# Kernel tuning notes

Measured on AMD Instinct MI355X. Metric: run time of the kernel, lower is better.

Reference implementation:

```python
import jax, jax.numpy as jnp
import numpy as np

BETA = 1.0 - 0.01      # 1 - voltage_decay
THRESH = 1.0           # threshold_voltage; theta state is never updated in the
                       # original forward (theta1/theta2 stay at init=0), so the
                       # effective adaptive threshold is THRESH + 0 every step.
ALPHA = 2.0            # snntorch default ATan surrogate alpha

@jax.custom_vjp
def spike_fn(x):
    # Heaviside forward, ATan surrogate backward (snntorch default spike_grad)
    return (x > 0).astype(x.dtype)

def _spike_fwd(x):
    return (x > 0).astype(x.dtype), x

def _spike_bwd(x, g):
    return (g * (ALPHA / 2.0) / (1.0 + (jnp.pi / 2.0 * ALPHA * x) ** 2),)

spike_fn.defvjp(_spike_fwd, _spike_bwd)

def setup_inputs() -> dict:
    key = jax.random.key(0)
    k0, k1, k2 = jax.random.split(key, 3)
    B, T, D, H, A = 128, 32, 6400, 1000, 4
    x = jax.random.normal(k0, (B, T, D), jnp.float32)
    W1 = jax.random.normal(k1, (H, D), jnp.float32) * (1.0 / np.sqrt(D))
    b1 = jnp.zeros((H,), jnp.float32)
    W2 = jax.random.normal(k2, (A, H), jnp.float32) * (1.0 / np.sqrt(H))
    b2 = jnp.zeros((A,), jnp.float32)
    return {"x": x, "W1": W1, "b1": b1, "W2": W2, "b2": b2}

def _lif_step(mem, cur, thr):
    # snntorch Leaky, reset_mechanism='zero':
    #   reset based on PREVIOUS mem crossing threshold (detached),
    #   zeroes the whole new state (leaked mem + input) on reset step.
    reset = jax.lax.stop_gradient((mem > thr).astype(mem.dtype))
    mem_new = (BETA * mem + cur) * (1.0 - reset)
    spk = spike_fn(mem_new - thr)
    return spk, mem_new

def _snn_forward(x, W1, b1, W2, b2):
    B, T, _ = x.shape
    H, A = W1.shape[0], W2.shape[0]

    def step(carry, cur):
        mem1, mem2 = carry
        h1 = cur @ W1.T + b1                 # [B,H]
        spk1, mem1 = _lif_step(mem1, h1, THRESH)
        h2 = spk1 @ W2.T + b2                # [B,A]
        spk2, mem2 = _lif_step(mem2, h2, THRESH)
        return (mem1, mem2), spk2

    init = (jnp.zeros((B, H), x.dtype), jnp.zeros((B, A), x.dtype))
    xt = jnp.swapaxes(x, 0, 1)               # [T,B,D]
    _, spk2_rec = jax.lax.scan(step, init, xt)
    return jnp.swapaxes(spk2_rec, 0, 1)      # [B,T,A]

def reference(x, W1, b1, W2, b2):
    return _snn_forward(x, W1, b1, W2, b2)
```

## Files before the change

kernel.cpp:

```cpp
#include <hip/hip_runtime.h>
#include <hip/hip_bf16.h>

constexpr int Bn = 128;
constexpr int Tn = 32;
constexpr int Dn = 6400;
constexpr int Hn = 1000;
constexpr int An = 4;
constexpr int Mn = Bn * Tn;
constexpr int Npad = 1024;

constexpr int KS = Dn / 32;
constexpr int MC = Mn / 16;
constexpr int NC = Npad / 16;

typedef _Float16 half8 __attribute__((ext_vector_type(8)));
typedef float floatx4 __attribute__((ext_vector_type(4)));

constexpr size_t H1_BYTES  = (size_t)Mn * Hn * 4;
constexpr size_t XS_BYTES  = (size_t)Mn * Dn * 2;
constexpr size_t WSp_BYTES = (size_t)Npad * Dn * 2;
constexpr size_t WS_NEEDED = H1_BYTES + 2 * XS_BYTES + 2 * WSp_BYTES;

__device__ __forceinline__ void async16(const void* g, void* l) {
    __builtin_amdgcn_global_load_lds(
        (const __attribute__((address_space(1))) void*)g,
        (__attribute__((address_space(3))) void*)l, 16, 0, 0);
}

__global__ __launch_bounds__(256)
void cvt_frag(const float* __restrict__ X, const float* __restrict__ W1,
              _Float16* __restrict__ Xh, _Float16* __restrict__ Xl,
              _Float16* __restrict__ Wh, _Float16* __restrict__ Wl)
{
    constexpr size_t nX8 = (size_t)Mn * Dn / 8;
    constexpr size_t nW8 = (size_t)Npad * Dn / 8;
    const size_t i = (size_t)blockIdx.x * 256 + threadIdx.x;

    float v[8];
    if (i < nX8) {
        const int c = (int)(i >> 6), l = (int)(i & 63);
        const int ks = c >> 8, m4 = c & (MC - 1);
        const int m = m4 * 16 + (l & 15);
        const int k = ks * 32 + ((l >> 4) & 3) * 8;
        const float4 v0 = *(const float4*)(X + (size_t)m * Dn + k);
        const float4 v1 = *(const float4*)(X + (size_t)m * Dn + k + 4);
        *(float4*)&v[0] = v0; *(float4*)&v[4] = v1;
        half8 hi, lo;
#pragma unroll
        for (int j = 0; j < 8; ++j) {
            hi[j] = (_Float16)v[j];
            lo[j] = (_Float16)((v[j] - (float)hi[j]) * 4096.0f);
        }
        *(half8*)(Xh + i * 8) = hi;
        *(half8*)(Xl + i * 8) = lo;
    } else if (i < nX8 + nW8) {
        const size_t jx = i - nX8;
        const int c = (int)(jx >> 6), l = (int)(jx & 63);
        const int ks = c >> 6, n4 = c & (NC - 1);
        const int n = n4 * 16 + (l & 15);
        const int k = ks * 32 + ((l >> 4) & 3) * 8;
        if (n < Hn) {
            const float4 v0 = *(const float4*)(W1 + (size_t)n * Dn + k);
            const float4 v1 = *(const float4*)(W1 + (size_t)n * Dn + k + 4);
            *(float4*)&v[0] = v0; *(float4*)&v[4] = v1;
        } else {
#pragma unroll
            for (int j = 0; j < 8; ++j) v[j] = 0.f;
        }
        half8 hi, lo;
#pragma unroll
        for (int j = 0; j < 8; ++j) {
            hi[j] = (_Float16)v[j];
            lo[j] = (_Float16)((v[j] - (float)hi[j]) * 4096.0f);
        }
        *(half8*)(Wh + jx * 8) = hi;
        *(half8*)(Wl + jx * 8) = lo;
    }
}

__global__ __launch_bounds__(256, 1)
void gemm_frag(const _Float16* __restrict__ Xh, const _Float16* __restrict__ Xl,
               const _Float16* __restrict__ Wh, const _Float16* __restrict__ Wl,
               const float* __restrict__ b1, float* __restrict__ H1)
{
    __shared__ __align__(16) _Float16 S[2][4][8][512];

    const int tid = threadIdx.x;
    const int lane = tid & 63;
    const int w = tid >> 6;
    const int nb = blockIdx.x & 7;
    const int mb = blockIdx.x >> 3;
    const int bm4 = mb * 8;
    const int bn4 = nb * 8;
    const int wm = w & 1;
    const int wn = w >> 1;

    auto issue = [&](int ks, int buf) {
#pragma unroll
        for (int r = 0; r < 2; ++r) {
            const int i = w * 2 + r;
            const size_t ga = ((size_t)(ks * MC + bm4 + i)) * 512 + lane * 8;
            const size_t gb = ((size_t)(ks * NC + bn4 + i)) * 512 + lane * 8;
            async16(Xh + ga, &S[buf][0][i][0]);
            async16(Xl + ga, &S[buf][1][i][0]);
            async16(Wh + gb, &S[buf][2][i][0]);
            async16(Wl + gb, &S[buf][3][i][0]);
        }
    };

    floatx4 acc0[4][4] = {};
    floatx4 acc1[4][4] = {};

    issue(0, 0);
    for (int it = 0; it < KS; ++it) {
        const int buf = it & 1;
        __syncthreads();
        if (it + 1 < KS) issue(it + 1, buf ^ 1);

        half8 ah[4], al[4], bh[4], bl[4];
#pragma unroll
        for (int mt = 0; mt < 4; ++mt) {
            ah[mt] = *(const half8*)&S[buf][0][wm * 4 + mt][lane * 8];
            al[mt] = *(const half8*)&S[buf][1][wm * 4 + mt][lane * 8];
        }
#pragma unroll
        for (int nt = 0; nt < 4; ++nt) {
            bh[nt] = *(const half8*)&S[buf][2][wn * 4 + nt][lane * 8];
            bl[nt] = *(const half8*)&S[buf][3][wn * 4 + nt][lane * 8];
        }
#pragma unroll
        for (int mt = 0; mt < 4; ++mt)
#pragma unroll
            for (int nt = 0; nt < 4; ++nt) {
                acc0[mt][nt] = __builtin_amdgcn_mfma_f32_16x16x32_f16(ah[mt], bh[nt], acc0[mt][nt], 0, 0, 0);
                acc1[mt][nt] = __builtin_amdgcn_mfma_f32_16x16x32_f16(ah[mt], bl[nt], acc1[mt][nt], 0, 0, 0);
                acc1[mt][nt] = __builtin_amdgcn_mfma_f32_16x16x32_f16(al[mt], bh[nt], acc1[mt][nt], 0, 0, 0);
            }
    }

    const int fr = lane & 15;
    const int fq = lane >> 4;
#pragma unroll
    for (int nt = 0; nt < 4; ++nt) {
        const int n = nb * 128 + wn * 64 + nt * 16 + fr;
        if (n >= Hn) continue;
        const float bias = b1[n];
#pragma unroll
        for (int mt = 0; mt < 4; ++mt) {
            const int m = mb * 128 + wm * 64 + mt * 16 + fq * 4;
#pragma unroll
            for (int r = 0; r < 4; ++r)
                H1[(size_t)(m + r) * Hn + n] =
                    acc0[mt][nt][r] + acc1[mt][nt][r] * (1.0f / 4096.0f) + bias;
        }
    }
}

__global__ __launch_bounds__(256, 4)
void gemm_fb(const float* __restrict__ X, const float* __restrict__ W1,
             const float* __restrict__ b1, float* __restrict__ H1)
{
    constexpr int K = Dn;
    constexpr int LD = 72;
    __shared__ __align__(16) _Float16 As[2][64][LD];
    __shared__ __align__(16) _Float16 Bs[2][64][LD];

    const int tid = threadIdx.x;
    const int bm = blockIdx.x * 64;
    const int bn = blockIdx.y * 64;
    const int lane = tid & 63;
    const int wid = tid >> 6;
    const int wm = (wid & 1) * 32;
    const int wn = (wid >> 1) * 32;
    const int fr = lane & 15;
    const int fq = lane >> 4;

    const int row0 = tid >> 3;
    const int row1 = (tid + 256) >> 3;
    const int k8_0 = (tid & 7) * 8;

    float4 rx[2][2], rw[2][2];
    const float zero4[4] = {0.f, 0.f, 0.f, 0.f};

    auto load_tiles = [&](int k0) {
        rx[0][0] = *(const float4*)(X + (size_t)(bm + row0) * K + k0 + k8_0);
        rx[0][1] = *(const float4*)(X + (size_t)(bm + row0) * K + k0 + k8_0 + 4);
        rx[1][0] = *(const float4*)(X + (size_t)(bm + row1) * K + k0 + k8_0);
        rx[1][1] = *(const float4*)(X + (size_t)(bm + row1) * K + k0 + k8_0 + 4);
        const int n0 = bn + row0, n1 = bn + row1;
        if (n0 < Hn) {
            rw[0][0] = *(const float4*)(W1 + (size_t)n0 * K + k0 + k8_0);
            rw[0][1] = *(const float4*)(W1 + (size_t)n0 * K + k0 + k8_0 + 4);
        } else { rw[0][0] = *(const float4*)zero4; rw[0][1] = *(const float4*)zero4; }
        if (n1 < Hn) {
            rw[1][0] = *(const float4*)(W1 + (size_t)n1 * K + k0 + k8_0);
            rw[1][1] = *(const float4*)(W1 + (size_t)n1 * K + k0 + k8_0 + 4);
        } else { rw[1][0] = *(const float4*)zero4; rw[1][1] = *(const float4*)zero4; }
    };

    load_tiles(0);
    floatx4 acc0[2][2] = {};
    floatx4 acc1[2][2] = {};

    for (int k0 = 0; k0 < K; k0 += 64) {
#pragma unroll
        for (int p = 0; p < 2; ++p) {
            const int row = p ? row1 : row0;
            float v[8];
            *(float4*)&v[0] = rx[p][0]; *(float4*)&v[4] = rx[p][1];
            half8 hi, lo;
#pragma unroll
            for (int j = 0; j < 8; ++j) {
                hi[j] = (_Float16)v[j];
                lo[j] = (_Float16)((v[j] - (float)hi[j]) * 4096.0f);
            }
            *(half8*)&As[0][row][k8_0] = hi;
            *(half8*)&As[1][row][k8_0] = lo;

            *(float4*)&v[0] = rw[p][0]; *(float4*)&v[4] = rw[p][1];
#pragma unroll
            for (int j = 0; j < 8; ++j) {
                hi[j] = (_Float16)v[j];
                lo[j] = (_Float16)((v[j] - (float)hi[j]) * 4096.0f);
            }
            *(half8*)&Bs[0][row][k8_0] = hi;
            *(half8*)&Bs[1][row][k8_0] = lo;
        }
        __syncthreads();
        if (k0 + 64 < K) load_tiles(k0 + 64);

#pragma unroll
        for (int c = 0; c < 2; ++c) {
            half8 ahi[2], alo[2], bhi[2], blo[2];
#pragma unroll
            for (int mt = 0; mt < 2; ++mt) {
                ahi[mt] = *(const half8*)&As[0][wm + mt * 16 + fr][c * 32 + fq * 8];
                alo[mt] = *(const half8*)&As[1][wm + mt * 16 + fr][c * 32 + fq * 8];
            }
#pragma unroll
            for (int nt = 0; nt < 2; ++nt) {
                bhi[nt] = *(const half8*)&Bs[0][wn + nt * 16 + fr][c * 32 + fq * 8];
                blo[nt] = *(const half8*)&Bs[1][wn + nt * 16 + fr][c * 32 + fq * 8];
            }
#pragma unroll
            for (int mt = 0; mt < 2; ++mt)
#pragma unroll
                for (int nt = 0; nt < 2; ++nt) {
                    acc0[mt][nt] = __builtin_amdgcn_mfma_f32_16x16x32_f16(ahi[mt], bhi[nt], acc0[mt][nt], 0, 0, 0);
                    acc1[mt][nt] = __builtin_amdgcn_mfma_f32_16x16x32_f16(ahi[mt], blo[nt], acc1[mt][nt], 0, 0, 0);
                    acc1[mt][nt] = __builtin_amdgcn_mfma_f32_16x16x32_f16(alo[mt], bhi[nt], acc1[mt][nt], 0, 0, 0);
                }
        }
        __syncthreads();
    }

#pragma unroll
    for (int nt = 0; nt < 2; ++nt) {
        const int n = bn + wn + nt * 16 + fr;
        if (n >= Hn) continue;
        const float bias = b1[n];
#pragma unroll
        for (int mt = 0; mt < 2; ++mt) {
            const int m = bm + wm + mt * 16 + fq * 4;
#pragma unroll
            for (int r = 0; r < 4; ++r)
                H1[(size_t)(m + r) * Hn + n] =
                    acc0[mt][nt][r] + acc1[mt][nt][r] * (1.0f / 4096.0f) + bias;
        }
    }
}

__global__ __launch_bounds__(1024)
void snn_scan(const float* __restrict__ H1, const float* __restrict__ W2,
              const float* __restrict__ b2, float* __restrict__ out)
{
    const int b = blockIdx.x;
    const int tid = threadIdx.x;
    const int lane = tid & 63;
    const int wid = tid >> 6;
    const bool act = (tid < Hn);

    __shared__ float w2s[1024][5];
    __shared__ unsigned smask[1024];
    __shared__ float h2s[Tn][An];

#pragma unroll
    for (int a = 0; a < An; ++a)
        w2s[tid][a] = act ? W2[a * Hn + tid] : 0.f;

    float cur[Tn];
#pragma unroll
    for (int t = 0; t < Tn; ++t)
        cur[t] = act ? H1[((size_t)b * Tn + t) * Hn + tid] : 0.f;

    unsigned mask = 0;
    float mem1 = 0.f;
#pragma unroll
    for (int t = 0; t < Tn; ++t) {
        const float reset = (mem1 > 1.0f) ? 1.0f : 0.0f;
        mem1 = (0.99f * mem1 + cur[t]) * (1.0f - reset);
        if (mem1 > 1.0f) mask |= (1u << t);
    }
    smask[tid] = mask;
    __syncthreads();

#pragma unroll
    for (int tt = 0; tt < 2; ++tt) {
        const int t = wid * 2 + tt;
        float p[An] = {0.f, 0.f, 0.f, 0.f};
        for (int h = lane; h < 1024; h += 64) {
            const float g = (smask[h] >> t) & 1u ? 1.0f : 0.0f;
#pragma unroll
            for (int a = 0; a < An; ++a) p[a] += g * w2s[h][a];
        }
#pragma unroll
        for (int off = 32; off > 0; off >>= 1)
#pragma unroll
            for (int a = 0; a < An; ++a) p[a] += __shfl_down(p[a], off, 64);
        if (lane == 0) {
#pragma unroll
            for (int a = 0; a < An; ++a) h2s[t][a] = p[a];
        }
    }
    __syncthreads();

    if (tid < An) {
        const float bias = b2[tid];
        float mem2 = 0.f;
#pragma unroll
        for (int t = 0; t < Tn; ++t) {
            const float h2 = h2s[t][tid] + bias;
            const float reset = (mem2 > 1.0f) ? 1.0f : 0.0f;
            mem2 = (0.99f * mem2 + h2) * (1.0f - reset);
            out[((size_t)b * Tn + t) * An + tid] = (mem2 > 1.0f) ? 1.0f : 0.0f;
        }
    }
}

extern "C" void kernel_launch(void* const* d_in, const int* in_sizes, int n_in,
                              void* d_out, int out_size, void* d_ws, size_t ws_size,
                              hipStream_t stream) {
    const float* x  = (const float*)d_in[0];
    const float* W1 = (const float*)d_in[1];
    const float* b1 = (const float*)d_in[2];
    const float* W2 = (const float*)d_in[3];
    const float* b2 = (const float*)d_in[4];
    float* out = (float*)d_out;

    char* ws = (char*)d_ws;
    float* H1 = (float*)ws;

    if (ws_size >= WS_NEEDED) {
        _Float16* Xh = (_Float16*)(ws + H1_BYTES);
        _Float16* Xl = (_Float16*)(ws + H1_BYTES + XS_BYTES);
        _Float16* Wh = (_Float16*)(ws + H1_BYTES + 2 * XS_BYTES);
        _Float16* Wl = (_Float16*)(ws + H1_BYTES + 2 * XS_BYTES + WSp_BYTES);

        constexpr size_t n8 = ((size_t)Mn * Dn + (size_t)Npad * Dn) / 8;
        cvt_frag<<<(unsigned)((n8 + 255) / 256), 256, 0, stream>>>(x, W1, Xh, Xl, Wh, Wl);

        gemm_frag<<<256, 256, 0, stream>>>(Xh, Xl, Wh, Wl, b1, H1);
    } else {
        dim3 grid(Mn / 64, (Hn + 63) / 64);
        gemm_fb<<<grid, 256, 0, stream>>>(x, W1, b1, H1);
    }
    snn_scan<<<Bn, 1024, 0, stream>>>(H1, W2, b2, out);
}
```

Measured before the change: 397.2 us.

## Replace LDS-staged split-fp16 GEMM with direct register-loaded MFMA GEMM

The fp16 hi/lo conversion now writes an interleaved row-major layout (32 hi then 32 lo per 32-element k-chunk), and the GEMM skips LDS entirely. Each wave loads its MFMA fragments straight from global memory into registers, double-buffered in software. Tiles shrink to 128x64 per block with 512 blocks and 2 blocks per CU. This removes the LDS staging and the per-step __syncthreads. The trade-off is that fragments shared between waves get no reuse, so global and L2 traffic rise and latency hiding depends on register prefetch.

Result: slower. 736.6 us (+85.4%).

```diff
diff --git a/kernel.cpp b/kernel.cpp
--- a/kernel.cpp
+++ b/kernel.cpp
@@ -10,144 +10,134 @@
 constexpr int Npad = 1024;
 
 constexpr int KS = Dn / 32;
-constexpr int MC = Mn / 16;
-constexpr int NC = Npad / 16;
 
 typedef _Float16 half8 __attribute__((ext_vector_type(8)));
 typedef float floatx4 __attribute__((ext_vector_type(4)));
 
 constexpr size_t H1_BYTES  = (size_t)Mn * Hn * 4;
-constexpr size_t XS_BYTES  = (size_t)Mn * Dn * 2;
-constexpr size_t WSp_BYTES = (size_t)Npad * Dn * 2;
-constexpr size_t WS_NEEDED = H1_BYTES + 2 * XS_BYTES + 2 * WSp_BYTES;
-
-__device__ __forceinline__ void async16(const void* g, void* l) {
-    __builtin_amdgcn_global_load_lds(
-        (const __attribute__((address_space(1))) void*)g,
-        (__attribute__((address_space(3))) void*)l, 16, 0, 0);
-}
+constexpr size_t XP_BYTES  = (size_t)Mn * Dn * 4;
+constexpr size_t WP_BYTES  = (size_t)Npad * Dn * 4;
+constexpr size_t WS_NEEDED = H1_BYTES + XP_BYTES + WP_BYTES;
 
 __global__ __launch_bounds__(256)
-void cvt_frag(const float* __restrict__ X, const float* __restrict__ W1,
-              _Float16* __restrict__ Xh, _Float16* __restrict__ Xl,
-              _Float16* __restrict__ Wh, _Float16* __restrict__ Wl)
+void cvt_pair(const float* __restrict__ X, const float* __restrict__ W1,
+              _Float16* __restrict__ Xp, _Float16* __restrict__ Wp)
 {
-    constexpr size_t nX8 = (size_t)Mn * Dn / 8;
-    constexpr size_t nW8 = (size_t)Npad * Dn / 8;
+    constexpr size_t nXg = (size_t)Mn * Dn / 32;
+    constexpr size_t nWg = (size_t)Npad * Dn / 32;
+    constexpr size_t nWreal = (size_t)Hn * KS;
     const size_t i = (size_t)blockIdx.x * 256 + threadIdx.x;
 
-    float v[8];
-    if (i < nX8) {
-        const int c = (int)(i >> 6), l = (int)(i & 63);
-        const int ks = c >> 8, m4 = c & (MC - 1);
-        const int m = m4 * 16 + (l & 15);
-        const int k = ks * 32 + ((l >> 4) & 3) * 8;
-        const float4 v0 = *(const float4*)(X + (size_t)m * Dn + k);
-        const float4 v1 = *(const float4*)(X + (size_t)m * Dn + k + 4);
-        *(float4*)&v[0] = v0; *(float4*)&v[4] = v1;
-        half8 hi, lo;
+    float v[32];
+    _Float16* dst;
+    if (i < nXg) {
+        const float* src = X + i * 32;
+#pragma unroll
+        for (int j = 0; j < 8; ++j) *(float4*)&v[j * 4] = *(const float4*)(src + j * 4);
+        dst = Xp + i * 64;
+    } else if (i < nXg + nWg) {
+        const size_t j = i - nXg;
+        if (j < nWreal) {
+            const float* src = W1 + j * 32;
+#pragma unroll
+            for (int q = 0; q < 8; ++q) *(float4*)&v[q * 4] = *(const float4*)(src + q * 4);
+        } else {
+#pragma unroll
+            for (int q = 0; q < 32; ++q) v[q] = 0.f;
+        }
+        dst = Wp + j * 64;
+    } else {
+        return;
+    }
+
+    half8 hi[4], lo[4];
+#pragma unroll
+    for (int g = 0; g < 4; ++g)
 #pragma unroll
         for (int j = 0; j < 8; ++j) {
-            hi[j] = (_Float16)v[j];
-            lo[j] = (_Float16)((v[j] - (float)hi[j]) * 4096.0f);
-        }
-        *(half8*)(Xh + i * 8) = hi;
-        *(half8*)(Xl + i * 8) = lo;
-    } else if (i < nX8 + nW8) {
-        const size_t jx = i - nX8;
-        const int c = (int)(jx >> 6), l = (int)(jx & 63);
-        const int ks = c >> 6, n4 = c & (NC - 1);
-        const int n = n4 * 16 + (l & 15);
-        const int k = ks * 32 + ((l >> 4) & 3) * 8;
-        if (n < Hn) {
-            const float4 v0 = *(const float4*)(W1 + (size_t)n * Dn + k);
-            const float4 v1 = *(const float4*)(W1 + (size_t)n * Dn + k + 4);
-            *(float4*)&v[0] = v0; *(float4*)&v[4] = v1;
-        } else {
-#pragma unroll
-            for (int j = 0; j < 8; ++j) v[j] = 0.f;
-        }
-        half8 hi, lo;
-#pragma unroll
-        for (int j = 0; j < 8; ++j) {
-            hi[j] = (_Float16)v[j];
-            lo[j] = (_Float16)((v[j] - (float)hi[j]) * 4096.0f);
-        }
-        *(half8*)(Wh + jx * 8) = hi;
-        *(half8*)(Wl + jx * 8) = lo;
-    }
-}
-
-__global__ __launch_bounds__(256, 1)
-void gemm_frag(const _Float16* __restrict__ Xh, const _Float16* __restrict__ Xl,
-               const _Float16* __restrict__ Wh, const _Float16* __restrict__ Wl,
-               const float* __restrict__ b1, float* __restrict__ H1)
+            const float f = v[g * 8 + j];
+            hi[g][j] = (_Float16)f;
+            lo[g][j] = (_Float16)((f - (float)hi[g][j]) * 4096.0f);
+        }
+#pragma unroll
+    for (int g = 0; g < 4; ++g) *(half8*)(dst + g * 8) = hi[g];
+#pragma unroll
+    for (int g = 0; g < 4; ++g) *(half8*)(dst + 32 + g * 8) = lo[g];
+}
+
+__global__ __launch_bounds__(256, 2)
+void gemm_direct(const _Float16* __restrict__ Xp, const _Float16* __restrict__ Wp,
+                 const float* __restrict__ b1, float* __restrict__ H1)
 {
-    __shared__ __align__(16) _Float16 S[2][4][8][512];
-
     const int tid = threadIdx.x;
     const int lane = tid & 63;
     const int w = tid >> 6;
-    const int nb = blockIdx.x & 7;
-    const int mb = blockIdx.x >> 3;
-    const int bm4 = mb * 8;
-    const int bn4 = nb * 8;
-    const int wm = w & 1;
-    const int wn = w >> 1;
-
-    auto issue = [&](int ks, int buf) {
-#pragma unroll
-        for (int r = 0; r < 2; ++r) {
-            const int i = w * 2 + r;
-            const size_t ga = ((size_t)(ks * MC + bm4 + i)) * 512 + lane * 8;
-            const size_t gb = ((size_t)(ks * NC + bn4 + i)) * 512 + lane * 8;
-            async16(Xh + ga, &S[buf][0][i][0]);
-            async16(Xl + ga, &S[buf][1][i][0]);
-            async16(Wh + gb, &S[buf][2][i][0]);
-            async16(Wl + gb, &S[buf][3][i][0]);
-        }
-    };
-
-    floatx4 acc0[4][4] = {};
-    floatx4 acc1[4][4] = {};
-
-    issue(0, 0);
-    for (int it = 0; it < KS; ++it) {
-        const int buf = it & 1;
-        __syncthreads();
-        if (it + 1 < KS) issue(it + 1, buf ^ 1);
-
-        half8 ah[4], al[4], bh[4], bl[4];
-#pragma unroll
-        for (int mt = 0; mt < 4; ++mt) {
-            ah[mt] = *(const half8*)&S[buf][0][wm * 4 + mt][lane * 8];
-            al[mt] = *(const half8*)&S[buf][1][wm * 4 + mt][lane * 8];
-        }
-#pragma unroll
-        for (int nt = 0; nt < 4; ++nt) {
-            bh[nt] = *(const half8*)&S[buf][2][wn * 4 + nt][lane * 8];
-            bl[nt] = *(const half8*)&S[buf][3][wn * 4 + nt][lane * 8];
-        }
-#pragma unroll
-        for (int mt = 0; mt < 4; ++mt)
-#pragma unroll
-            for (int nt = 0; nt < 4; ++nt) {
-                acc0[mt][nt] = __builtin_amdgcn_mfma_f32_16x16x32_f16(ah[mt], bh[nt], acc0[mt][nt], 0, 0, 0);
-                acc1[mt][nt] = __builtin_amdgcn_mfma_f32_16x16x32_f16(ah[mt], bl[nt], acc1[mt][nt], 0, 0, 0);
-                acc1[mt][nt] = __builtin_amdgcn_mfma_f32_16x16x32_f16(al[mt], bh[nt], acc1[mt][nt], 0, 0, 0);
-            }
-    }
-
+    const int nb = blockIdx.x & 15;
+    const int mb = blockIdx.x >> 4;
+    const int wm = (w & 1) * 64;
+    const int wn = (w >> 1) * 32;
     const int fr = lane & 15;
-    const int fq = lane >> 4;
-#pragma unroll
-    for (int nt = 0; nt < 4; ++nt) {
-        const int n = nb * 128 + wn * 64 + nt * 16 + fr;
+    const int kg = lane >> 4;
+
+    const _Float16* abase[4];
+    const _Float16* bbase[2];
+#pragma unroll
+    for (int mt = 0; mt < 4; ++mt)
+        abase[mt] = Xp + (size_t)(mb * 128 + wm + mt * 16 + fr) * (KS * 64) + kg * 8;
+#pragma unroll
+    for (int nt = 0; nt < 2; ++nt)
+        bbase[nt] = Wp + (size_t)(nb * 64 + wn + nt * 16 + fr) * (KS * 64) + kg * 8;
+
+    half8 fa[2][4][2], fb[2][2][2];
+    floatx4 acc0[4][2] = {};
+    floatx4 acc1[4][2] = {};
+
+#define LOADF(ks, p)                                                          \
+    {                                                                         \
+        const size_t o = (size_t)(ks) * 64;                                   \
+        _Pragma("unroll") for (int mt = 0; mt < 4; ++mt) {                    \
+            fa[p][mt][0] = *(const half8*)(abase[mt] + o);                    \
+            fa[p][mt][1] = *(const half8*)(abase[mt] + o + 32);               \
+        }                                                                     \
+        _Pragma("unroll") for (int nt = 0; nt < 2; ++nt) {                    \
+            fb[p][nt][0] = *(const half8*)(bbase[nt] + o);                    \
+            fb[p][nt][1] = *(const half8*)(bbase[nt] + o + 32);               \
+        }                                                                     \
+    }
+
+#define COMPUTE(p)                                                            \
+    _Pragma("unroll") for (int mt = 0; mt < 4; ++mt)                          \
+        _Pragma("unroll") for (int nt = 0; nt < 2; ++nt) {                    \
+            acc0[mt][nt] = __builtin_amdgcn_mfma_f32_16x16x32_f16(            \
+                fa[p][mt][0], fb[p][nt][0], acc0[mt][nt], 0, 0, 0);           \
+            acc1[mt][nt] = __builtin_amdgcn_mfma_f32_16x16x32_f16(            \
+                fa[p][mt][0], fb[p][nt][1], acc1[mt][nt], 0, 0, 0);           \
+            acc1[mt][nt] = __builtin_amdgcn_mfma_f32_16x16x32_f16(            \
+                fa[p][mt][1], fb[p][nt][0], acc1[mt][nt], 0, 0, 0);           \
+        }
+
+    LOADF(0, 0)
+#pragma unroll 1
+    for (int it = 0; it < KS - 2; it += 2) {
+        LOADF(it + 1, 1)
+        COMPUTE(0)
+        LOADF(it + 2, 0)
+        COMPUTE(1)
+    }
+    LOADF(KS - 1, 1)
+    COMPUTE(0)
+    COMPUTE(1)
+#undef LOADF
+#undef COMPUTE
+
+#pragma unroll
+    for (int nt = 0; nt < 2; ++nt) {
+        const int n = nb * 64 + wn + nt * 16 + fr;
         if (n >= Hn) continue;
         const float bias = b1[n];
 #pragma unroll
         for (int mt = 0; mt < 4; ++mt) {
-            const int m = mb * 128 + wm * 64 + mt * 16 + fq * 4;
+            const int m = mb * 128 + wm + mt * 16 + kg * 4;
 #pragma unroll
             for (int r = 0; r < 4; ++r)
                 H1[(size_t)(m + r) * Hn + n] =
@@ -351,15 +341,13 @@
     float* H1 = (float*)ws;
 
     if (ws_size >= WS_NEEDED) {
-        _Float16* Xh = (_Float16*)(ws + H1_BYTES);
-        _Float16* Xl = (_Float16*)(ws + H1_BYTES + XS_BYTES);
-        _Float16* Wh = (_Float16*)(ws + H1_BYTES + 2 * XS_BYTES);
-        _Float16* Wl = (_Float16*)(ws + H1_BYTES + 2 * XS_BYTES + WSp_BYTES);
-
-        constexpr size_t n8 = ((size_t)Mn * Dn + (size_t)Npad * Dn) / 8;
-        cvt_frag<<<(unsigned)((n8 + 255) / 256), 256, 0, stream>>>(x, W1, Xh, Xl, Wh, Wl);
-
-        gemm_frag<<<256, 256, 0, stream>>>(Xh, Xl, Wh, Wl, b1, H1);
+        _Float16* Xp = (_Float16*)(ws + H1_BYTES);
+        _Float16* Wp = (_Float16*)(ws + H1_BYTES + XP_BYTES);
+
+        constexpr size_t ng = ((size_t)Mn * Dn + (size_t)Npad * Dn) / 32;
+        cvt_pair<<<(unsigned)((ng + 255) / 256), 256, 0, stream>>>(x, W1, Xp, Wp);
+
+        gemm_direct<<<512, 256, 0, stream>>>(Xp, Wp, b1, H1);
     } else {
         dim3 grid(Mn / 64, (Hn + 63) / 64);
         gemm_fb<<<grid, 256, 0, stream>>>(x, W1, b1, H1);
```

## Coalesce fp16 split conversion via LDS transpose and halve GEMM N-tile

Applied to the files above, without the earlier changes.

Rewrites the fp32-to-split-fp16 conversion so each block reads contiguous row segments with coalesced float4 loads. It stages them in padded LDS and then writes them out in MFMA fragment order, replacing the scattered strided reads of the old per-fragment layout. The GEMM tile shrinks from 128x128 to 128x64 per block, giving 512 blocks with 2 blocks per CU allowed. The aim is better occupancy and latency hiding, paid for with more reloads of the A operand.

New measurement: 366.7 us. 1.08x faster.

```diff
diff --git a/kernel.cpp b/kernel.cpp
--- a/kernel.cpp
+++ b/kernel.cpp
@@ -14,6 +14,7 @@
 constexpr int NC = Npad / 16;
 
 typedef _Float16 half8 __attribute__((ext_vector_type(8)));
+typedef _Float16 half4 __attribute__((ext_vector_type(4)));
 typedef float floatx4 __attribute__((ext_vector_type(4)));
 
 constexpr size_t H1_BYTES  = (size_t)Mn * Hn * 4;
@@ -28,88 +29,98 @@
 }
 
 __global__ __launch_bounds__(256)
-void cvt_frag(const float* __restrict__ X, const float* __restrict__ W1,
-              _Float16* __restrict__ Xh, _Float16* __restrict__ Xl,
-              _Float16* __restrict__ Wh, _Float16* __restrict__ Wl)
+void cvt2(const float* __restrict__ X, const float* __restrict__ W1,
+          _Float16* __restrict__ Xh, _Float16* __restrict__ Xl,
+          _Float16* __restrict__ Wh, _Float16* __restrict__ Wl)
 {
-    constexpr size_t nX8 = (size_t)Mn * Dn / 8;
-    constexpr size_t nW8 = (size_t)Npad * Dn / 8;
-    const size_t i = (size_t)blockIdx.x * 256 + threadIdx.x;
-
-    float v[8];
-    if (i < nX8) {
-        const int c = (int)(i >> 6), l = (int)(i & 63);
-        const int ks = c >> 8, m4 = c & (MC - 1);
-        const int m = m4 * 16 + (l & 15);
-        const int k = ks * 32 + ((l >> 4) & 3) * 8;
-        const float4 v0 = *(const float4*)(X + (size_t)m * Dn + k);
-        const float4 v1 = *(const float4*)(X + (size_t)m * Dn + k + 4);
-        *(float4*)&v[0] = v0; *(float4*)&v[4] = v1;
-        half8 hi, lo;
-#pragma unroll
-        for (int j = 0; j < 8; ++j) {
-            hi[j] = (_Float16)v[j];
-            lo[j] = (_Float16)((v[j] - (float)hi[j]) * 4096.0f);
-        }
-        *(half8*)(Xh + i * 8) = hi;
-        *(half8*)(Xl + i * 8) = lo;
-    } else if (i < nX8 + nW8) {
-        const size_t jx = i - nX8;
-        const int c = (int)(jx >> 6), l = (int)(jx & 63);
-        const int ks = c >> 6, n4 = c & (NC - 1);
-        const int n = n4 * 16 + (l & 15);
-        const int k = ks * 32 + ((l >> 4) & 3) * 8;
-        if (n < Hn) {
-            const float4 v0 = *(const float4*)(W1 + (size_t)n * Dn + k);
-            const float4 v1 = *(const float4*)(W1 + (size_t)n * Dn + k + 4);
-            *(float4*)&v[0] = v0; *(float4*)&v[4] = v1;
-        } else {
-#pragma unroll
-            for (int j = 0; j < 8; ++j) v[j] = 0.f;
-        }
-        half8 hi, lo;
-#pragma unroll
-        for (int j = 0; j < 8; ++j) {
-            hi[j] = (_Float16)v[j];
-            lo[j] = (_Float16)((v[j] - (float)hi[j]) * 4096.0f);
-        }
-        *(half8*)(Wh + jx * 8) = hi;
-        *(half8*)(Wl + jx * 8) = lo;
-    }
-}
-
-__global__ __launch_bounds__(256, 1)
-void gemm_frag(const _Float16* __restrict__ Xh, const _Float16* __restrict__ Xl,
-               const _Float16* __restrict__ Wh, const _Float16* __restrict__ Wl,
-               const float* __restrict__ b1, float* __restrict__ H1)
-{
-    __shared__ __align__(16) _Float16 S[2][4][8][512];
+    constexpr int LD2 = 264;
+    __shared__ __align__(16) _Float16 hiS[16][LD2];
+    __shared__ __align__(16) _Float16 loS[16][LD2];
 
     const int tid = threadIdx.x;
     const int lane = tid & 63;
     const int w = tid >> 6;
-    const int nb = blockIdx.x & 7;
-    const int mb = blockIdx.x >> 3;
+    const int bx = blockIdx.x;
+
+    const float* src;
+    _Float16 *dh, *dl;
+    int c4, ks0, crow, nrows;
+    if (bx < 256 * 25) {
+        c4 = bx & 255; ks0 = (bx >> 8) * 8;
+        src = X; dh = Xh; dl = Xl; crow = MC; nrows = 16;
+    } else {
+        const int b2 = bx - 256 * 25;
+        c4 = b2 & 63; ks0 = (b2 >> 6) * 8;
+        src = W1; dh = Wh; dl = Wl; crow = NC; nrows = Hn - c4 * 16;
+    }
+
+#pragma unroll
+    for (int j = 0; j < 4; ++j) {
+        const int row = w * 4 + j;
+        float4 v = make_float4(0.f, 0.f, 0.f, 0.f);
+        if (row < nrows)
+            v = *(const float4*)(src + (size_t)(c4 * 16 + row) * Dn + ks0 * 32 + lane * 4);
+        half4 hi, lo;
+        hi[0] = (_Float16)v.x; lo[0] = (_Float16)((v.x - (float)hi[0]) * 4096.0f);
+        hi[1] = (_Float16)v.y; lo[1] = (_Float16)((v.y - (float)hi[1]) * 4096.0f);
+        hi[2] = (_Float16)v.z; lo[2] = (_Float16)((v.z - (float)hi[2]) * 4096.0f);
+        hi[3] = (_Float16)v.w; lo[3] = (_Float16)((v.w - (float)hi[3]) * 4096.0f);
+        *(half4*)&hiS[row][lane * 4] = hi;
+        *(half4*)&loS[row][lane * 4] = lo;
+    }
+    __syncthreads();
+
+    const int lr = lane & 15, lg = lane >> 4;
+#pragma unroll
+    for (int q = 0; q < 2; ++q) {
+        const int ks = w * 2 + q;
+        const size_t cbase = ((size_t)(ks0 + ks) * crow + c4) * 512;
+        const half8 h = *(const half8*)&hiS[lr][ks * 32 + lg * 8];
+        const half8 l = *(const half8*)&loS[lr][ks * 32 + lg * 8];
+        *(half8*)(dh + cbase + lane * 8) = h;
+        *(half8*)(dl + cbase + lane * 8) = l;
+    }
+}
+
+constexpr int AH = 0;
+constexpr int AL = 8 * 512;
+constexpr int BH = 16 * 512;
+constexpr int BL = 20 * 512;
+constexpr int BUFSZ = 24 * 512;
+
+__global__ __launch_bounds__(256, 2)
+void gemm_frag2(const _Float16* __restrict__ Xh, const _Float16* __restrict__ Xl,
+                const _Float16* __restrict__ Wh, const _Float16* __restrict__ Wl,
+                const float* __restrict__ b1, float* __restrict__ H1)
+{
+    __shared__ __align__(16) _Float16 S[2 * BUFSZ];
+
+    const int tid = threadIdx.x;
+    const int lane = tid & 63;
+    const int w = tid >> 6;
+    const int nb = blockIdx.x & 15;
+    const int mb = blockIdx.x >> 4;
     const int bm4 = mb * 8;
-    const int bn4 = nb * 8;
+    const int bn4 = nb * 4;
     const int wm = w & 1;
     const int wn = w >> 1;
 
     auto issue = [&](int ks, int buf) {
+        _Float16* base = &S[buf * BUFSZ];
 #pragma unroll
         for (int r = 0; r < 2; ++r) {
             const int i = w * 2 + r;
             const size_t ga = ((size_t)(ks * MC + bm4 + i)) * 512 + lane * 8;
-            const size_t gb = ((size_t)(ks * NC + bn4 + i)) * 512 + lane * 8;
-            async16(Xh + ga, &S[buf][0][i][0]);
-            async16(Xl + ga, &S[buf][1][i][0]);
-            async16(Wh + gb, &S[buf][2][i][0]);
-            async16(Wl + gb, &S[buf][3][i][0]);
-        }
+            async16(Xh + ga, base + AH + i * 512);
+            async16(Xl + ga, base + AL + i * 512);
+        }
+        const size_t gb = ((size_t)(ks * NC + bn4 + w)) * 512 + lane * 8;
+        async16(Wh + gb, base + BH + w * 512);
+        async16(Wl + gb, base + BL + w * 512);
     };
 
-    floatx4 acc0[4][4] = {};
-    floatx4 acc1[4][4] = {};
+    floatx4 acc0[4][2] = {};
+    floatx4 acc1[4][2] = {};
 
     issue(0, 0);
     for (int it = 0; it < KS; ++it) {
@@ -117,21 +128,22 @@
         __syncthreads();
         if (it + 1 < KS) issue(it + 1, buf ^ 1);
 
-        half8 ah[4], al[4], bh[4], bl[4];
+        const _Float16* base = &S[buf * BUFSZ];
+        half8 ah[4], al[4], bh[2], bl[2];
 #pragma unroll
         for (int mt = 0; mt < 4; ++mt) {
-            ah[mt] = *(const half8*)&S[buf][0][wm * 4 + mt][lane * 8];
-            al[mt] = *(const half8*)&S[buf][1][wm * 4 + mt][lane * 8];
-        }
-#pragma unroll
-        for (int nt = 0; nt < 4; ++nt) {
-            bh[nt] = *(const half8*)&S[buf][2][wn * 4 + nt][lane * 8];
-            bl[nt] = *(const half8*)&S[buf][3][wn * 4 + nt][lane * 8];
+            ah[mt] = *(const half8*)(base + AH + (wm * 4 + mt) * 512 + lane * 8);
+            al[mt] = *(const half8*)(base + AL + (wm * 4 + mt) * 512 + lane * 8);
+        }
+#pragma unroll
+        for (int nt = 0; nt < 2; ++nt) {
+            bh[nt] = *(const half8*)(base + BH + (wn * 2 + nt) * 512 + lane * 8);
+            bl[nt] = *(const half8*)(base + BL + (wn * 2 + nt) * 512 + lane * 8);
         }
 #pragma unroll
         for (int mt = 0; mt < 4; ++mt)
 #pragma unroll
-            for (int nt = 0; nt < 4; ++nt) {
+            for (int nt = 0; nt < 2; ++nt) {
                 acc0[mt][nt] = __builtin_amdgcn_mfma_f32_16x16x32_f16(ah[mt], bh[nt], acc0[mt][nt], 0, 0, 0);
                 acc1[mt][nt] = __builtin_amdgcn_mfma_f32_16x16x32_f16(ah[mt], bl[nt], acc1[mt][nt], 0, 0, 0);
                 acc1[mt][nt] = __builtin_amdgcn_mfma_f32_16x16x32_f16(al[mt], bh[nt], acc1[mt][nt], 0, 0, 0);
@@ -141,8 +153,8 @@
     const int fr = lane & 15;
     const int fq = lane >> 4;
 #pragma unroll
-    for (int nt = 0; nt < 4; ++nt) {
-        const int n = nb * 128 + wn * 64 + nt * 16 + fr;
+    for (int nt = 0; nt < 2; ++nt) {
+        const int n = nb * 64 + wn * 32 + nt * 16 + fr;
         if (n >= Hn) continue;
         const float bias = b1[n];
 #pragma unroll
@@ -356,10 +368,8 @@
         _Float16* Wh = (_Float16*)(ws + H1_BYTES + 2 * XS_BYTES);
         _Float16* Wl = (_Float16*)(ws + H1_BYTES + 2 * XS_BYTES + WSp_BYTES);
 
-        constexpr size_t n8 = ((size_t)Mn * Dn + (size_t)Npad * Dn) / 8;
-        cvt_frag<<<(unsigned)((n8 + 255) / 256), 256, 0, stream>>>(x, W1, Xh, Xl, Wh, Wl);
-
-        gemm_frag<<<256, 256, 0, stream>>>(Xh, Xl, Wh, Wl, b1, H1);
+        cvt2<<<256 * 25 + 64 * 25, 256, 0, stream>>>(x, W1, Xh, Xl, Wh, Wl);
+        gemm_frag2<<<512, 256, 0, stream>>>(Xh, Xl, Wh, Wl, b1, H1);
     } else {
         dim3 grid(Mn / 64, (Hn + 63) / 64);
         gemm_fb<<<grid, 256, 0, stream>>>(x, W1, b1, H1);
```
